# Kernel optimization log

Hardware: AMD Instinct MI355X
Metric: run time of the kernel (lower is better)

## Reference

```python
import jax, jax.numpy as jnp
import numpy as np

B, S, DK = 32, 2048, 64

def setup_inputs() -> dict:
    key = jax.random.key(0)
    kq, kk, kv = jax.random.split(key, 3)
    Q = jax.random.normal(kq, (B, S, DK), dtype=jnp.float32)
    K = jax.random.normal(kk, (B, S, DK), dtype=jnp.float32)
    V = jax.random.normal(kv, (B, S, DK), dtype=jnp.float32)
    return {"Q": Q, "K": K, "V": V}

def reference(Q, K, V):
    # attn_scores = Q K^T / sqrt(d_k); full [B,S,S] probs materialized (naive, non-flash)
    d_k = Q.shape[-1]
    scores = jnp.einsum('bqd,bkd->bqk', Q, K) / jnp.sqrt(jnp.asarray(d_k, Q.dtype))
    probs = jax.nn.softmax(scores, axis=-1)
    return jnp.einsum('bqk,bkd->bqd', probs, V)
```

## Files before the change

### kernel.cpp

```cpp
#include <hip/hip_runtime.h>
#include <hip/hip_bf16.h>

#define BATCH 32
#define SEQ   2048
#define DKK   64

constexpr int QT  = 128;
constexpr int KT  = 128;
constexpr int NIT = SEQ / KT;
constexpr int LSK = 66;
constexpr int LSV = 130;

typedef __attribute__((ext_vector_type(8)))  short bf16x8;
typedef __attribute__((ext_vector_type(16))) float f32x16;
typedef __attribute__((ext_vector_type(2)))  unsigned uint2v;

__device__ __forceinline__ unsigned cvt2(float a, float b) {
    union { __hip_bfloat162 h; unsigned u; } c;
    c.h = __float22bfloat162_rn(make_float2(a, b));
    return c.u;
}

__device__ __forceinline__ unsigned short b16u(float x) {
    union { __hip_bfloat16 h; unsigned short u; } t;
    t.h = __float2bfloat16(x);
    return t.u;
}

__device__ __forceinline__ float fast_exp2(float x) {
#if __has_builtin(__builtin_amdgcn_exp2f)
    return __builtin_amdgcn_exp2f(x);
#else
    return exp2f(x);
#endif
}

__global__ __launch_bounds__(256) void prep_kv(
        const float* __restrict__ K, const float* __restrict__ V,
        unsigned short* __restrict__ K16, unsigned short* __restrict__ V16) {
    __shared__ unsigned short T[64][66];
    const int b   = blockIdx.y;
    const int k0  = blockIdx.x << 6;
    const int tid = threadIdx.x;
    const int r   = tid >> 2;
    const int c   = (tid & 3) << 4;

    {
        const float* kp = K + ((size_t)b * SEQ + k0 + r) * DKK + c;
        float4 a0 = *(const float4*)(kp + 0);
        float4 a1 = *(const float4*)(kp + 4);
        float4 a2 = *(const float4*)(kp + 8);
        float4 a3 = *(const float4*)(kp + 12);
        union { bf16x8 v; unsigned u[4]; } w0, w1;
        w0.u[0] = cvt2(a0.x, a0.y); w0.u[1] = cvt2(a0.z, a0.w);
        w0.u[2] = cvt2(a1.x, a1.y); w0.u[3] = cvt2(a1.z, a1.w);
        w1.u[0] = cvt2(a2.x, a2.y); w1.u[1] = cvt2(a2.z, a2.w);
        w1.u[2] = cvt2(a3.x, a3.y); w1.u[3] = cvt2(a3.z, a3.w);
        unsigned short* kd = K16 + ((size_t)b * SEQ + k0 + r) * DKK + c;
        *(bf16x8*)(kd)     = w0.v;
        *(bf16x8*)(kd + 8) = w1.v;
    }
    {
        const float* vp = V + ((size_t)b * SEQ + k0 + r) * DKK + c;
        float4 a0 = *(const float4*)(vp + 0);
        float4 a1 = *(const float4*)(vp + 4);
        float4 a2 = *(const float4*)(vp + 8);
        float4 a3 = *(const float4*)(vp + 12);
        const float f[16] = {a0.x,a0.y,a0.z,a0.w, a1.x,a1.y,a1.z,a1.w,
                             a2.x,a2.y,a2.z,a2.w, a3.x,a3.y,a3.z,a3.w};
        #pragma unroll
        for (int j = 0; j < 16; ++j) T[c + j][r] = b16u(f[j]);
        __syncthreads();
        unsigned short* vd = V16 + ((size_t)b * DKK + r) * SEQ + k0 + c;
        union { bf16x8 v; unsigned short s[8]; } o0, o1;
        #pragma unroll
        for (int j = 0; j < 8; ++j) { o0.s[j] = T[r][c + j]; o1.s[j] = T[r][c + 8 + j]; }
        *(bf16x8*)(vd)     = o0.v;
        *(bf16x8*)(vd + 8) = o1.v;
    }
}

__global__ __launch_bounds__(256, 2) void attn_fwd(
        const float* __restrict__ Q, const unsigned short* __restrict__ K16,
        const unsigned short* __restrict__ V16, float* __restrict__ O) {
    __shared__ short Kb[2][KT][LSK];
    __shared__ short Vt[2][DKK][LSV];

    const int tid  = threadIdx.x;
    const int w    = tid >> 6;
    const int lane = tid & 63;
    const int hi   = lane >> 5;
    const int l31  = lane & 31;

    const int lin  = (int)blockIdx.x + ((int)blockIdx.y << 4);
    const int work = ((lin & 7) << 6) | (lin >> 3);
    const int b    = work >> 4;
    const int q0   = (work & 15) * QT + w * 32;

    const float qscale = 0.125f * 1.44269504088896340736f;
    bf16x8 qfrag[4];
    #pragma unroll
    for (int c = 0; c < 4; ++c) {
        const float* qp = Q + ((size_t)b * SEQ + q0 + l31) * DKK + 16*c + 8*hi;
        float4 a  = *(const float4*)qp;
        float4 a2 = *(const float4*)(qp + 4);
        union { bf16x8 v; unsigned u[4]; } f;
        f.u[0] = cvt2(a.x*qscale,  a.y*qscale);
        f.u[1] = cvt2(a.z*qscale,  a.w*qscale);
        f.u[2] = cvt2(a2.x*qscale, a2.y*qscale);
        f.u[3] = cvt2(a2.z*qscale, a2.w*qscale);
        qfrag[c] = f.v;
    }

    f32x16 o0a = {}, o0b = {}, o1a = {}, o1b = {};
    float ls0 = 0.f, ls1 = 0.f, ls2 = 0.f, ls3 = 0.f;

    const unsigned short* Kbase = K16 + (size_t)b * SEQ * DKK;
    const unsigned short* Vbase = V16 + (size_t)b * DKK * SEQ;

    const int sr = tid >> 3;
    const int sc = (tid & 7) << 3;

    bf16x8 kreg[4], vreg[4];
    auto load_regs = [&](int t) {
        const unsigned short* Kg = Kbase + (size_t)(t * KT) * DKK + sc;
        #pragma unroll
        for (int i = 0; i < 4; ++i)
            kreg[i] = *(const bf16x8*)(Kg + (size_t)(sr + 32*i) * DKK);
        const unsigned short* Vg = Vbase + (size_t)sr * SEQ + t * KT + sc;
        #pragma unroll
        for (int i = 0; i < 2; ++i) {
            vreg[2*i]     = *(const bf16x8*)(Vg + (size_t)(32*i) * SEQ);
            vreg[2*i + 1] = *(const bf16x8*)(Vg + (size_t)(32*i) * SEQ + 64);
        }
    };
    auto write_lds = [&](int buf) {
        #pragma unroll
        for (int i = 0; i < 4; ++i)
            *(bf16x8*)&Kb[buf][sr + 32*i][sc] = kreg[i];
        #pragma unroll
        for (int i = 0; i < 2; ++i) {
            *(bf16x8*)&Vt[buf][sr + 32*i][sc]      = vreg[2*i];
            *(bf16x8*)&Vt[buf][sr + 32*i][sc + 64] = vreg[2*i + 1];
        }
    };

    auto qk = [&](int buf, int n) {
        f32x16 a = {};
        #pragma unroll
        for (int cd = 0; cd < 4; ++cd) {
            bf16x8 kf = *(const bf16x8*)&Kb[buf][32*n + l31][16*cd + 8*hi];
            a = __builtin_amdgcn_mfma_f32_32x32x16_bf16(kf, qfrag[cd], a, 0, 0, 0);
        }
        return a;
    };
    auto ldvf = [&](int buf, int n, bf16x8* vf) {
        #pragma unroll
        for (int cc = 0; cc < 2; ++cc) {
            const int c = 2*n + cc;
            vf[2*cc]     = *(const bf16x8*)&Vt[buf][l31     ][16*c + 8*hi];
            vf[2*cc + 1] = *(const bf16x8*)&Vt[buf][32 + l31][16*c + 8*hi];
        }
    };
    auto smpack = [&](const f32x16& acc, bf16x8& pa0v, bf16x8& pa1v) {
        float p[16];
        #pragma unroll
        for (int r = 0; r < 16; r += 4) {
            p[r]   = fast_exp2(acc[r]);   ls0 += p[r];
            p[r+1] = fast_exp2(acc[r+1]); ls1 += p[r+1];
            p[r+2] = fast_exp2(acc[r+2]); ls2 += p[r+2];
            p[r+3] = fast_exp2(acc[r+3]); ls3 += p[r+3];
        }
        unsigned pw0 = cvt2(p[0],  p[1]),  pw1 = cvt2(p[2],  p[3]);
        unsigned pw2 = cvt2(p[4],  p[5]),  pw3 = cvt2(p[6],  p[7]);
        unsigned pw4 = cvt2(p[8],  p[9]),  pw5 = cvt2(p[10], p[11]);
        unsigned pw6 = cvt2(p[12], p[13]), pw7 = cvt2(p[14], p[15]);
        uint2v s02 = __builtin_amdgcn_permlane32_swap(pw0, pw2, false, false);
        uint2v s13 = __builtin_amdgcn_permlane32_swap(pw1, pw3, false, false);
        uint2v s46 = __builtin_amdgcn_permlane32_swap(pw4, pw6, false, false);
        uint2v s57 = __builtin_amdgcn_permlane32_swap(pw5, pw7, false, false);
        union { bf16x8 v; unsigned u[4]; } pa0, pa1;
        pa0.u[0] = s02[0]; pa0.u[1] = s13[0]; pa0.u[2] = s02[1]; pa0.u[3] = s13[1];
        pa1.u[0] = s46[0]; pa1.u[1] = s57[0]; pa1.u[2] = s46[1]; pa1.u[3] = s57[1];
        pa0v = pa0.v; pa1v = pa1.v;
    };
    auto pv = [&](bf16x8 pa0v, bf16x8 pa1v, const bf16x8* vf) {
        o0a = __builtin_amdgcn_mfma_f32_32x32x16_bf16(vf[0], pa0v, o0a, 0, 0, 0);
        o1a = __builtin_amdgcn_mfma_f32_32x32x16_bf16(vf[1], pa0v, o1a, 0, 0, 0);
        o0b = __builtin_amdgcn_mfma_f32_32x32x16_bf16(vf[2], pa1v, o0b, 0, 0, 0);
        o1b = __builtin_amdgcn_mfma_f32_32x32x16_bf16(vf[3], pa1v, o1b, 0, 0, 0);
    };

    load_regs(0);
    write_lds(0);
    load_regs(1);
    __syncthreads();

    f32x16 accA, accB;
    bf16x8 vA[4], vB[4], pa0, pa1;
    accA = qk(0, 0); ldvf(0, 0, vA);
    accB = qk(0, 1); ldvf(0, 1, vB);

    for (int it = 0; it < NIT; ++it) {
        const int cur = it & 1;
        const int nxt = cur ^ 1;

        smpack(accA, pa0, pa1); pv(pa0, pa1, vA);
        accA = qk(cur, 2); ldvf(cur, 2, vA);
        smpack(accB, pa0, pa1); pv(pa0, pa1, vB);
        accB = qk(cur, 3); ldvf(cur, 3, vB);

        if (it + 1 < NIT) {
            write_lds(nxt);
            if (it + 2 < NIT) load_regs(it + 2);
            asm volatile("s_waitcnt lgkmcnt(0)" ::: "memory");
            __builtin_amdgcn_s_barrier();

            smpack(accA, pa0, pa1); pv(pa0, pa1, vA);
            accA = qk(nxt, 0); ldvf(nxt, 0, vA);
            smpack(accB, pa0, pa1); pv(pa0, pa1, vB);
            accB = qk(nxt, 1); ldvf(nxt, 1, vB);
        } else {
            smpack(accA, pa0, pa1); pv(pa0, pa1, vA);
            smpack(accB, pa0, pa1); pv(pa0, pa1, vB);
        }
    }

    float s = (ls0 + ls1) + (ls2 + ls3);
    s += __shfl_xor(s, 32);
    const float inv = 1.0f / s;

    float* op = O + ((size_t)b * SEQ + q0 + l31) * DKK;
    #pragma unroll
    for (int G = 0; G < 4; ++G) {
        float4 st;
        st.x = (o0a[4*G + 0] + o0b[4*G + 0]) * inv;
        st.y = (o0a[4*G + 1] + o0b[4*G + 1]) * inv;
        st.z = (o0a[4*G + 2] + o0b[4*G + 2]) * inv;
        st.w = (o0a[4*G + 3] + o0b[4*G + 3]) * inv;
        *(float4*)(op + 8*G + 4*hi) = st;
        st.x = (o1a[4*G + 0] + o1b[4*G + 0]) * inv;
        st.y = (o1a[4*G + 1] + o1b[4*G + 1]) * inv;
        st.z = (o1a[4*G + 2] + o1b[4*G + 2]) * inv;
        st.w = (o1a[4*G + 3] + o1b[4*G + 3]) * inv;
        *(float4*)(op + 32 + 8*G + 4*hi) = st;
    }
}

extern "C" void kernel_launch(void* const* d_in, const int* in_sizes, int n_in,
                              void* d_out, int out_size, void* d_ws, size_t ws_size,
                              hipStream_t stream) {
    const float* Q = (const float*)d_in[0];
    const float* K = (const float*)d_in[1];
    const float* V = (const float*)d_in[2];
    float* O = (float*)d_out;

    unsigned short* K16 = (unsigned short*)d_ws;
    unsigned short* V16 = K16 + (size_t)BATCH * SEQ * DKK;

    prep_kv<<<dim3(SEQ / 64, BATCH), dim3(256), 0, stream>>>(K, V, K16, V16);
    dim3 grid(SEQ / QT, BATCH);
    attn_fwd<<<grid, dim3(256), 0, stream>>>(Q, K16, V16, O);
}
```

Before: 137.4 us.

## Load K/V fragments directly from global into registers, dropping LDS staging

```diff
diff --git a/kernel.cpp b/kernel.cpp
--- a/kernel.cpp
+++ b/kernel.cpp
@@ -5,11 +5,7 @@
 #define SEQ   2048
 #define DKK   64
 
-constexpr int QT  = 128;
-constexpr int KT  = 128;
-constexpr int NIT = SEQ / KT;
-constexpr int LSK = 66;
-constexpr int LSV = 130;
+constexpr int NHT = SEQ / 32;
 
 typedef __attribute__((ext_vector_type(8)))  short bf16x8;
 typedef __attribute__((ext_vector_type(16))) float f32x16;
@@ -83,9 +79,6 @@
 __global__ __launch_bounds__(256, 2) void attn_fwd(
         const float* __restrict__ Q, const unsigned short* __restrict__ K16,
         const unsigned short* __restrict__ V16, float* __restrict__ O) {
-    __shared__ short Kb[2][KT][LSK];
-    __shared__ short Vt[2][DKK][LSV];
-
     const int tid  = threadIdx.x;
     const int w    = tid >> 6;
     const int lane = tid & 63;
@@ -95,7 +88,7 @@
     const int lin  = (int)blockIdx.x + ((int)blockIdx.y << 4);
     const int work = ((lin & 7) << 6) | (lin >> 3);
     const int b    = work >> 4;
-    const int q0   = (work & 15) * QT + w * 32;
+    const int q0   = (work & 15) * 128 + w * 32;
 
     const float qscale = 0.125f * 1.44269504088896340736f;
     bf16x8 qfrag[4];
@@ -115,52 +108,30 @@
     f32x16 o0a = {}, o0b = {}, o1a = {}, o1b = {};
     float ls0 = 0.f, ls1 = 0.f, ls2 = 0.f, ls3 = 0.f;
 
-    const unsigned short* Kbase = K16 + (size_t)b * SEQ * DKK;
-    const unsigned short* Vbase = V16 + (size_t)b * DKK * SEQ;
-
-    const int sr = tid >> 3;
-    const int sc = (tid & 7) << 3;
-
-    bf16x8 kreg[4], vreg[4];
-    auto load_regs = [&](int t) {
-        const unsigned short* Kg = Kbase + (size_t)(t * KT) * DKK + sc;
-        #pragma unroll
-        for (int i = 0; i < 4; ++i)
-            kreg[i] = *(const bf16x8*)(Kg + (size_t)(sr + 32*i) * DKK);
-        const unsigned short* Vg = Vbase + (size_t)sr * SEQ + t * KT + sc;
-        #pragma unroll
-        for (int i = 0; i < 2; ++i) {
-            vreg[2*i]     = *(const bf16x8*)(Vg + (size_t)(32*i) * SEQ);
-            vreg[2*i + 1] = *(const bf16x8*)(Vg + (size_t)(32*i) * SEQ + 64);
-        }
-    };
-    auto write_lds = [&](int buf) {
-        #pragma unroll
-        for (int i = 0; i < 4; ++i)
-            *(bf16x8*)&Kb[buf][sr + 32*i][sc] = kreg[i];
-        #pragma unroll
-        for (int i = 0; i < 2; ++i) {
-            *(bf16x8*)&Vt[buf][sr + 32*i][sc]      = vreg[2*i];
-            *(bf16x8*)&Vt[buf][sr + 32*i][sc + 64] = vreg[2*i + 1];
-        }
-    };
-
-    auto qk = [&](int buf, int n) {
+    const unsigned short* Kb_ = K16 + (size_t)b * SEQ * DKK;
+    const unsigned short* Vb_ = V16 + (size_t)b * DKK * SEQ;
+
+    auto ldk = [&](int ht, bf16x8* k) {
+        const unsigned short* p = Kb_ + (size_t)(32*ht + l31) * DKK + 8*hi;
+        k[0] = *(const bf16x8*)(p);
+        k[1] = *(const bf16x8*)(p + 16);
+        k[2] = *(const bf16x8*)(p + 32);
+        k[3] = *(const bf16x8*)(p + 48);
+    };
+    auto ldv = [&](int ht, bf16x8* v) {
+        const unsigned short* p0 = Vb_ + (size_t)l31        * SEQ + 32*ht + 8*hi;
+        const unsigned short* p1 = Vb_ + (size_t)(32 + l31) * SEQ + 32*ht + 8*hi;
+        v[0] = *(const bf16x8*)(p0);
+        v[1] = *(const bf16x8*)(p1);
+        v[2] = *(const bf16x8*)(p0 + 16);
+        v[3] = *(const bf16x8*)(p1 + 16);
+    };
+    auto qkm = [&](const bf16x8* k) {
         f32x16 a = {};
         #pragma unroll
-        for (int cd = 0; cd < 4; ++cd) {
-            bf16x8 kf = *(const bf16x8*)&Kb[buf][32*n + l31][16*cd + 8*hi];
-            a = __builtin_amdgcn_mfma_f32_32x32x16_bf16(kf, qfrag[cd], a, 0, 0, 0);
-        }
+        for (int cd = 0; cd < 4; ++cd)
+            a = __builtin_amdgcn_mfma_f32_32x32x16_bf16(k[cd], qfrag[cd], a, 0, 0, 0);
         return a;
-    };
-    auto ldvf = [&](int buf, int n, bf16x8* vf) {
-        #pragma unroll
-        for (int cc = 0; cc < 2; ++cc) {
-            const int c = 2*n + cc;
-            vf[2*cc]     = *(const bf16x8*)&Vt[buf][l31     ][16*c + 8*hi];
-            vf[2*cc + 1] = *(const bf16x8*)&Vt[buf][32 + l31][16*c + 8*hi];
-        }
     };
     auto smpack = [&](const f32x16& acc, bf16x8& pa0v, bf16x8& pa1v) {
         float p[16];
@@ -184,47 +155,36 @@
         pa1.u[0] = s46[0]; pa1.u[1] = s57[0]; pa1.u[2] = s46[1]; pa1.u[3] = s57[1];
         pa0v = pa0.v; pa1v = pa1.v;
     };
-    auto pv = [&](bf16x8 pa0v, bf16x8 pa1v, const bf16x8* vf) {
-        o0a = __builtin_amdgcn_mfma_f32_32x32x16_bf16(vf[0], pa0v, o0a, 0, 0, 0);
-        o1a = __builtin_amdgcn_mfma_f32_32x32x16_bf16(vf[1], pa0v, o1a, 0, 0, 0);
-        o0b = __builtin_amdgcn_mfma_f32_32x32x16_bf16(vf[2], pa1v, o0b, 0, 0, 0);
-        o1b = __builtin_amdgcn_mfma_f32_32x32x16_bf16(vf[3], pa1v, o1b, 0, 0, 0);
-    };
-
-    load_regs(0);
-    write_lds(0);
-    load_regs(1);
-    __syncthreads();
-
-    f32x16 accA, accB;
-    bf16x8 vA[4], vB[4], pa0, pa1;
-    accA = qk(0, 0); ldvf(0, 0, vA);
-    accB = qk(0, 1); ldvf(0, 1, vB);
-
-    for (int it = 0; it < NIT; ++it) {
-        const int cur = it & 1;
-        const int nxt = cur ^ 1;
-
-        smpack(accA, pa0, pa1); pv(pa0, pa1, vA);
-        accA = qk(cur, 2); ldvf(cur, 2, vA);
-        smpack(accB, pa0, pa1); pv(pa0, pa1, vB);
-        accB = qk(cur, 3); ldvf(cur, 3, vB);
-
-        if (it + 1 < NIT) {
-            write_lds(nxt);
-            if (it + 2 < NIT) load_regs(it + 2);
-            asm volatile("s_waitcnt lgkmcnt(0)" ::: "memory");
-            __builtin_amdgcn_s_barrier();
-
-            smpack(accA, pa0, pa1); pv(pa0, pa1, vA);
-            accA = qk(nxt, 0); ldvf(nxt, 0, vA);
-            smpack(accB, pa0, pa1); pv(pa0, pa1, vB);
-            accB = qk(nxt, 1); ldvf(nxt, 1, vB);
-        } else {
-            smpack(accA, pa0, pa1); pv(pa0, pa1, vA);
-            smpack(accB, pa0, pa1); pv(pa0, pa1, vB);
-        }
-    }
+    auto pv = [&](bf16x8 pa0v, bf16x8 pa1v, const bf16x8* v) {
+        o0a = __builtin_amdgcn_mfma_f32_32x32x16_bf16(v[0], pa0v, o0a, 0, 0, 0);
+        o1a = __builtin_amdgcn_mfma_f32_32x32x16_bf16(v[1], pa0v, o1a, 0, 0, 0);
+        o0b = __builtin_amdgcn_mfma_f32_32x32x16_bf16(v[2], pa1v, o0b, 0, 0, 0);
+        o1b = __builtin_amdgcn_mfma_f32_32x32x16_bf16(v[3], pa1v, o1b, 0, 0, 0);
+    };
+
+    bf16x8 kE[4], kO[4], vE[4], vO[4], pa0, pa1;
+    f32x16 accE, accO;
+
+    ldk(0, kE); ldk(1, kO); ldv(0, vE); ldv(1, vO);
+    accE = qkm(kE);
+    ldk(2, kE);
+    accO = qkm(kO);
+    ldk(3, kO);
+
+    for (int m = 0; m < 31; ++m) {
+        smpack(accE, pa0, pa1);
+        pv(pa0, pa1, vE);
+        ldv(2*m + 2, vE);
+        accE = qkm(kE);
+        ldk(2*m + 4 < NHT ? 2*m + 4 : NHT - 1, kE);
+        smpack(accO, pa0, pa1);
+        pv(pa0, pa1, vO);
+        ldv(2*m + 3, vO);
+        accO = qkm(kO);
+        ldk(2*m + 5 < NHT ? 2*m + 5 : NHT - 1, kO);
+    }
+    smpack(accE, pa0, pa1); pv(pa0, pa1, vE);
+    smpack(accO, pa0, pa1); pv(pa0, pa1, vO);
 
     float s = (ls0 + ls1) + (ls2 + ls3);
     s += __shfl_xor(s, 32);
@@ -259,6 +219,6 @@
     unsigned short* V16 = K16 + (size_t)BATCH * SEQ * DKK;
 
     prep_kv<<<dim3(SEQ / 64, BATCH), dim3(256), 0, stream>>>(K, V, K16, V16);
-    dim3 grid(SEQ / QT, BATCH);
+    dim3 grid(SEQ / 128, BATCH);
     attn_fwd<<<grid, dim3(256), 0, stream>>>(Q, K16, V16, O);
 }
```

Result: slower. 210.3 us (+53.1%).
